# Performance work log

Hardware: AMD Instinct MI355X
Metric: run time of the kernel (lower is better)

## Reference

```python
import jax, jax.numpy as jnp
import numpy as np

N_NODES = 100000
N_EDGES = 3200000
IN_DIM = 128
OUT_DIM = 128
BN_EPS = 1e-5
FILL_VALUE = 1.0  # improved_gcn=False -> self-loop weight 1.0 (2.0 if improved)


def setup_inputs() -> dict:
    key = jax.random.key(0)
    k1, k2, k3, k4 = jax.random.split(key, 4)
    node_features = jax.random.normal(k1, (N_NODES, IN_DIM), dtype=jnp.float32)
    edge_index = jax.random.randint(k2, (2, N_EDGES), 0, N_NODES, dtype=jnp.int64)
    edge_weight = jax.random.uniform(k3, (N_EDGES,), dtype=jnp.float32)
    # Glorot init like PyG GCNConv
    W = jax.random.normal(k4, (IN_DIM, OUT_DIM), dtype=jnp.float32) * np.sqrt(2.0 / (IN_DIM + OUT_DIM))
    b = jnp.zeros((OUT_DIM,), dtype=jnp.float32)
    gamma = jnp.ones((OUT_DIM,), dtype=jnp.float32)
    beta = jnp.zeros((OUT_DIM,), dtype=jnp.float32)
    return {"node_features": node_features, "edge_index": edge_index,
            "edge_weight": edge_weight, "W": W, "b": b, "gamma": gamma, "beta": beta}


def reference(node_features, edge_index, edge_weight, W, b, gamma, beta):
    N = node_features.shape[0]
    dt = node_features.dtype
    # --- gcn_norm: add self loops, symmetric normalization ---
    loop = jnp.arange(N, dtype=edge_index.dtype)
    row = jnp.concatenate([edge_index[0], loop])  # source
    col = jnp.concatenate([edge_index[1], loop])  # target (aggregation dim)
    w = jnp.concatenate([edge_weight.astype(dt), jnp.full((N,), FILL_VALUE, dtype=dt)])
    deg = jax.ops.segment_sum(w, col, num_segments=N)
    dinv = jnp.where(deg > 0, jax.lax.rsqrt(deg), 0.0).astype(dt)
    norm = dinv[row] * w * dinv[col]  # [E+N]
    # --- linear transform then message passing (scatter-add into targets) ---
    x = node_features @ W  # [N, out_dim]
    msg = x[row] * norm[:, None]  # [E+N, out_dim] gather
    out = jax.ops.segment_sum(msg, col, num_segments=N) + b
    # --- relu ---
    h = jax.nn.relu(out)
    # --- BatchNorm1d (training-mode batch statistics, biased variance) ---
    mean = jnp.mean(h, axis=0)
    var = jnp.mean(jnp.square(h - mean), axis=0)
    h = (h - mean) * jax.lax.rsqrt(var + BN_EPS) * gamma + beta
    # dropout is identity in eval / deterministic reference
    return h
```

## Files before the change

kernel.cpp:

```cpp
#include <hip/hip_runtime.h>
#include <hip/hip_bf16.h>


#define BKT_BITS 7
#define BKT_SZ 128
#define MAX_BKT 1024
#define CHUNK 8192

typedef __attribute__((ext_vector_type(8))) short bf16x8;
typedef __attribute__((ext_vector_type(4))) float f32x4;

__device__ __forceinline__ unsigned bf16rn(float f) {
    unsigned x = __float_as_uint(f);
    return (x + 0x7fffu + ((x >> 16) & 1u)) >> 16;
}
__device__ __forceinline__ float bflo(unsigned u) { return __uint_as_float(u << 16); }
__device__ __forceinline__ float bfhi(unsigned u) { return __uint_as_float(u & 0xffff0000u); }

__global__ __launch_bounds__(256) void k_bhist2(const int* __restrict__ col,
        int* __restrict__ blkoff, const float* __restrict__ Wm,
        unsigned* __restrict__ WT, int E, int nb, int nbc) {
    __shared__ int h[MAX_BKT];
    for (int i = threadIdx.x; i < nb; i += 256) h[i] = 0;
    __syncthreads();
    int base = blockIdx.x * CHUNK, lim = min(base + CHUNK, E);
    for (int e = base + threadIdx.x; e < lim; e += 256)
        atomicAdd(&h[col[e] >> BKT_BITS], 1);
    __syncthreads();
    for (int i = threadIdx.x; i < nb; i += 256)
        blkoff[(size_t)i * nbc + blockIdx.x] = h[i];
    if (blockIdx.x == 0) {
        for (int i = threadIdx.x; i < 128 * 64; i += 256) {
            int j = i >> 6, w = i & 63;
            float a = Wm[(size_t)(2 * w) * 128 + j];
            float b = Wm[(size_t)(2 * w + 1) * 128 + j];
            WT[i] = bf16rn(a) | (bf16rn(b) << 16);
        }
    }
}

__global__ void k_bscan2a(int* __restrict__ blkoff, int* __restrict__ btot,
                          int nb, int nbc) {
    int b = blockIdx.x * 256 + threadIdx.x;
    if (b >= nb) return;
    int* p = blkoff + (size_t)b * nbc;
    int run = 0;
#pragma unroll 4
    for (int i = 0; i < nbc; ++i) { int c = p[i]; p[i] = run; run += c; }
    btot[b] = run;
}

__global__ __launch_bounds__(1024) void k_bscan2b(const int* __restrict__ btot,
        int* __restrict__ bbase, int* __restrict__ ptr, float* __restrict__ sums,
        int nb, int N, int E) {
    __shared__ int ls[1024];
    int t = threadIdx.x;
    int v = (t < nb) ? btot[t] : 0;
    ls[t] = v;
    __syncthreads();
    for (int off = 1; off < 1024; off <<= 1) {
        int u = (t >= off) ? ls[t - off] : 0;
        __syncthreads();
        ls[t] += u;
        __syncthreads();
    }
    if (t < nb) bbase[t] = ls[t] - v;
    if (t == nb - 1) bbase[nb] = ls[t];
    if (t == 0) ptr[N] = E;
    if (t < 512) sums[t] = 0.0f;
}

__global__ __launch_bounds__(256) void k_passA3(
        const int* __restrict__ row, const int* __restrict__ col,
        const float* __restrict__ w, const int* __restrict__ blkoff,
        const int* __restrict__ bbase, unsigned* __restrict__ tmp,
        int E, int nb, int nbc) {
    __shared__ int cur[MAX_BKT];
    for (int i = threadIdx.x; i < nb; i += 256)
        cur[i] = bbase[i] + blkoff[(size_t)i * nbc + blockIdx.x];
    __syncthreads();
    int base = blockIdx.x * CHUNK, lim = min(base + CHUNK, E);
    for (int e = base + threadIdx.x; e < lim; e += 256) {
        int c = col[e];
        int q8 = (int)(w[e] * 256.0f + 0.5f);
        if (q8 > 255) q8 = 255;
        unsigned rec = ((unsigned)row[e] << 15) | ((unsigned)(c & 127) << 8) | (unsigned)q8;
        int pos = atomicAdd(&cur[c >> BKT_BITS], 1);
        tmp[pos] = rec;
    }
}

__global__ __launch_bounds__(256) void k_passB2(
        const unsigned* __restrict__ tmp, const int* __restrict__ bbase,
        unsigned* __restrict__ packed, int* __restrict__ ptr,
        float* __restrict__ dinv, int N) {
    __shared__ int hcnt[BKT_SZ];
    __shared__ int wsumi[BKT_SZ];
    __shared__ int cur[BKT_SZ];
    __shared__ float dcl[BKT_SZ];
    int b = blockIdx.x;
    int t = threadIdx.x;
    if (t < BKT_SZ) { hcnt[t] = 0; wsumi[t] = 0; }
    __syncthreads();
    int beg = bbase[b], end = bbase[b + 1];
    for (int k = beg + t; k < end; k += 256) {
        unsigned p = tmp[k];
        int li = (p >> 8) & 127;
        atomicAdd(&hcnt[li], 1);
        atomicAdd(&wsumi[li], (int)(p & 255u));
    }
    __syncthreads();
    if (t < BKT_SZ) cur[t] = hcnt[t];
    __syncthreads();
    for (int off = 1; off < BKT_SZ; off <<= 1) {
        int v = (t < BKT_SZ && t >= off) ? cur[t - off] : 0;
        __syncthreads();
        if (t < BKT_SZ) cur[t] += v;
        __syncthreads();
    }
    if (t < BKT_SZ) {
        int p = beg + cur[t] - hcnt[t];
        cur[t] = p;
        float d = 1.0f + (float)wsumi[t] * (1.0f / 256.0f);
        float dc = rsqrtf(d);
        dcl[t] = dc;
        int n = (b << BKT_BITS) + t;
        if (n < N) { ptr[n] = p; dinv[n] = dc; }
    }
    __syncthreads();
    for (int k = beg + t; k < end; k += 256) {
        unsigned p = tmp[k];
        int li = (p >> 8) & 127;
        int pos = atomicAdd(&cur[li], 1);
        float fw = (float)(p & 255u) * (1.0f / 256.0f) * dcl[li];
        unsigned wb = bf16rn(fw) & 0x7FFFu;
        packed[pos] = ((p >> 15) << 15) | wb;
    }
}

__global__ void k_conv2(const float* __restrict__ nf, const float* __restrict__ dinv,
                        uint4* __restrict__ tab, int N) {
    size_t i = (size_t)blockIdx.x * 256 + threadIdx.x;
    if (i >= (size_t)N * 16) return;
    int n = (int)(i >> 4);
    float dv = dinv[n];
    const float4* src = (const float4*)nf + 2 * i;
    float4 a = src[0], b = src[1];
    uint4 r;
    r.x = bf16rn(a.x * dv) | (bf16rn(a.y * dv) << 16);
    r.y = bf16rn(a.z * dv) | (bf16rn(a.w * dv) << 16);
    r.z = bf16rn(b.x * dv) | (bf16rn(b.y * dv) << 16);
    r.w = bf16rn(b.z * dv) | (bf16rn(b.w * dv) << 16);
    tab[i] = r;
}

#define EDGE_FMA(aX, nX, tX)                                     \
    aX[0] += nX * bflo(tX.x); aX[1] += nX * bfhi(tX.x);          \
    aX[2] += nX * bflo(tX.y); aX[3] += nX * bfhi(tX.y);          \
    aX[4] += nX * bflo(tX.z); aX[5] += nX * bfhi(tX.z);          \
    aX[6] += nX * bflo(tX.w); aX[7] += nX * bfhi(tX.w);

__global__ __launch_bounds__(256) void k_gatherw5(
        const unsigned* __restrict__ packed, const int* __restrict__ ptr,
        const float* __restrict__ dinv, const unsigned* __restrict__ tab,
        unsigned* __restrict__ aggb, int N) {
    int wid = (int)(((size_t)blockIdx.x * 256 + threadIdx.x) >> 6);
    int lane = threadIdx.x & 63;
    if (wid >= N) return;
    int beg = ptr[wid], end = ptr[wid + 1];
    float dc = dinv[wid];
    int q = lane >> 4;
    int fl = lane & 15;
    float a0[8] = {}, a1[8] = {}, a2[8] = {}, a3[8] = {};
    int k = beg;
    for (; k + 16 <= end; k += 16) {
        unsigned p0 = packed[k + q];
        unsigned p1 = packed[k + 4 + q];
        unsigned p2 = packed[k + 8 + q];
        unsigned p3 = packed[k + 12 + q];
        uint4 t0 = *(const uint4*)(tab + (size_t)(p0 >> 15) * 64 + fl * 4);
        uint4 t1 = *(const uint4*)(tab + (size_t)(p1 >> 15) * 64 + fl * 4);
        uint4 t2 = *(const uint4*)(tab + (size_t)(p2 >> 15) * 64 + fl * 4);
        uint4 t3 = *(const uint4*)(tab + (size_t)(p3 >> 15) * 64 + fl * 4);
        float n0 = bflo(p0 & 0x7FFFu);
        float n1 = bflo(p1 & 0x7FFFu);
        float n2 = bflo(p2 & 0x7FFFu);
        float n3 = bflo(p3 & 0x7FFFu);
        EDGE_FMA(a0, n0, t0)
        EDGE_FMA(a1, n1, t1)
        EDGE_FMA(a2, n2, t2)
        EDGE_FMA(a3, n3, t3)
    }
    if (k + 8 <= end) {
        unsigned p0 = packed[k + q];
        unsigned p1 = packed[k + 4 + q];
        uint4 t0 = *(const uint4*)(tab + (size_t)(p0 >> 15) * 64 + fl * 4);
        uint4 t1 = *(const uint4*)(tab + (size_t)(p1 >> 15) * 64 + fl * 4);
        float n0 = bflo(p0 & 0x7FFFu);
        float n1 = bflo(p1 & 0x7FFFu);
        EDGE_FMA(a0, n0, t0)
        EDGE_FMA(a1, n1, t1)
        k += 8;
    }
    for (; k < end; k += 4) {
        int i0 = k + q;
        if (i0 < end) {
            unsigned p0 = packed[i0];
            uint4 t0 = *(const uint4*)(tab + (size_t)(p0 >> 15) * 64 + fl * 4);
            float n0 = bflo(p0 & 0x7FFFu);
            EDGE_FMA(a0, n0, t0)
        }
    }
#pragma unroll
    for (int j = 0; j < 8; ++j) {
        float s = (a0[j] + a1[j]) + (a2[j] + a3[j]);
        s += __shfl_xor(s, 16);
        s += __shfl_xor(s, 32);
        a0[j] = s;
    }
    if (q == 0) {
        uint4 t = *(const uint4*)(tab + (size_t)wid * 64 + fl * 4);
        EDGE_FMA(a0, dc, t)
        uint4 r;
        r.x = bf16rn(a0[0]) | (bf16rn(a0[1]) << 16);
        r.y = bf16rn(a0[2]) | (bf16rn(a0[3]) << 16);
        r.z = bf16rn(a0[4]) | (bf16rn(a0[5]) << 16);
        r.w = bf16rn(a0[6]) | (bf16rn(a0[7]) << 16);
        *(uint4*)(aggb + (size_t)wid * 64 + fl * 4) = r;
    }
}

__global__ __launch_bounds__(256) void k_gatherwF(
        const unsigned* __restrict__ packed, const int* __restrict__ ptr,
        const float* __restrict__ dinv, const unsigned* __restrict__ tab,
        float* __restrict__ out, int N) {
    int wid = (int)(((size_t)blockIdx.x * 256 + threadIdx.x) >> 6);
    int lane = threadIdx.x & 63;
    if (wid >= N) return;
    int beg = ptr[wid], end = ptr[wid + 1];
    float dc = dinv[wid];
    int q = lane >> 4;
    int fl = lane & 15;
    float a0[8] = {}, a1[8] = {};
    int k = beg;
    for (; k + 8 <= end; k += 8) {
        unsigned p0 = packed[k + q];
        unsigned p1 = packed[k + 4 + q];
        uint4 t0 = *(const uint4*)(tab + (size_t)(p0 >> 15) * 64 + fl * 4);
        uint4 t1 = *(const uint4*)(tab + (size_t)(p1 >> 15) * 64 + fl * 4);
        float n0 = bflo(p0 & 0x7FFFu);
        float n1 = bflo(p1 & 0x7FFFu);
        EDGE_FMA(a0, n0, t0)
        EDGE_FMA(a1, n1, t1)
    }
    for (; k < end; k += 4) {
        int i0 = k + q;
        if (i0 < end) {
            unsigned p0 = packed[i0];
            uint4 t0 = *(const uint4*)(tab + (size_t)(p0 >> 15) * 64 + fl * 4);
            float n0 = bflo(p0 & 0x7FFFu);
            EDGE_FMA(a0, n0, t0)
        }
    }
#pragma unroll
    for (int j = 0; j < 8; ++j) {
        float s = a0[j] + a1[j];
        s += __shfl_xor(s, 16);
        s += __shfl_xor(s, 32);
        a0[j] = s;
    }
    if (q == 0) {
        uint4 t = *(const uint4*)(tab + (size_t)wid * 64 + fl * 4);
        EDGE_FMA(a0, dc, t)
        float4* dst = (float4*)(out + (size_t)wid * 128 + fl * 8);
        dst[0] = make_float4(a0[0], a0[1], a0[2], a0[3]);
        dst[1] = make_float4(a0[4], a0[5], a0[6], a0[7]);
    }
}

__global__ __launch_bounds__(256) void k_gemm4(
        unsigned* aggb, const unsigned* __restrict__ WT,
        const float* __restrict__ bias, float* __restrict__ sums, int N) {
    __shared__ unsigned A_l[128][68];
    __shared__ float bs[256];
    int tid = threadIdx.x;
    int r0 = blockIdx.x * 128;
    bs[tid] = 0.0f;
    {
        int j = tid >> 1, h = tid & 1;
        int gr = r0 + j;
        if (gr < N) {
            const uint4* src = (const uint4*)(aggb + (size_t)gr * 64 + h * 32);
#pragma unroll
            for (int i = 0; i < 8; ++i)
                *(uint4*)&A_l[j][h * 32 + i * 4] = src[i];
        } else {
            uint4 z = {0, 0, 0, 0};
#pragma unroll
            for (int i = 0; i < 8; ++i)
                *(uint4*)&A_l[j][h * 32 + i * 4] = z;
        }
    }
    __syncthreads();

    int wv = tid >> 6, l = tid & 63;
    int lr = l & 15, lk = l >> 4;
    f32x4 acc[2][8] = {};
#pragma unroll
    for (int ks = 0; ks < 4; ++ks) {
        bf16x8 a0 = *(bf16x8*)&A_l[wv * 32 + lr][ks * 16 + lk * 4];
        bf16x8 a1 = *(bf16x8*)&A_l[wv * 32 + 16 + lr][ks * 16 + lk * 4];
#pragma unroll
        for (int nt = 0; nt < 8; ++nt) {
            bf16x8 b = *(const bf16x8*)(WT + (size_t)(nt * 16 + lr) * 64 + ks * 16 + lk * 4);
            acc[0][nt] = __builtin_amdgcn_mfma_f32_16x16x32_bf16(a0, b, acc[0][nt], 0, 0, 0);
            acc[1][nt] = __builtin_amdgcn_mfma_f32_16x16x32_bf16(a1, b, acc[1][nt], 0, 0, 0);
        }
    }

    unsigned short* ab = (unsigned short*)aggb;
#pragma unroll
    for (int nt = 0; nt < 8; ++nt) {
        int colc = nt * 16 + lr;
        float bc = bias[colc];
        float s = 0.0f, sq = 0.0f;
#pragma unroll
        for (int ms = 0; ms < 2; ++ms) {
#pragma unroll
            for (int p = 0; p < 4; ++p) {
                int rrow = r0 + wv * 32 + ms * 16 + lk * 4 + p;
                float v = fmaxf(acc[ms][nt][p] + bc, 0.0f);
                if (rrow < N) {
                    ab[(size_t)rrow * 128 + colc] = (unsigned short)bf16rn(v);
                    s += v;
                    sq += v * v;
                }
            }
        }
        s += __shfl_xor(s, 16);  s += __shfl_xor(s, 32);
        sq += __shfl_xor(sq, 16); sq += __shfl_xor(sq, 32);
        if (l < 16) {
            atomicAdd(&bs[colc], s);
            atomicAdd(&bs[128 + colc], sq);
        }
    }
    __syncthreads();
    if (tid < 128) {
        atomicAdd(&sums[tid], bs[tid]);
        atomicAdd(&sums[128 + tid], bs[128 + tid]);
    }
}

__global__ __launch_bounds__(256) void k_bnapplyB2(
        const unsigned* __restrict__ aggb, const float* __restrict__ sums,
        const float* __restrict__ gamma, const float* __restrict__ beta,
        float* __restrict__ out, size_t n16, int N) {
    __shared__ float sc[128], sh[128];
    int t = threadIdx.x;
    if (t < 128) {
        float inv_n = 1.0f / (float)N;
        float mean = sums[t] * inv_n;
        float var = sums[128 + t] * inv_n - mean * mean;
        float s = rsqrtf(var + 1e-5f) * gamma[t];
        sc[t] = s;
        sh[t] = beta[t] - mean * s;
    }
    __syncthreads();
    size_t i = (size_t)blockIdx.x * 256 + threadIdx.x;
    if (i >= n16) return;
    int g = (int)(i & 15);
    uint4 v = ((const uint4*)aggb)[i];
    float4 sc0 = *(float4*)&sc[g * 8];
    float4 sc1 = *(float4*)&sc[g * 8 + 4];
    float4 sh0 = *(float4*)&sh[g * 8];
    float4 sh1 = *(float4*)&sh[g * 8 + 4];
    float4 o0, o1;
    o0.x = bflo(v.x) * sc0.x + sh0.x;
    o0.y = bfhi(v.x) * sc0.y + sh0.y;
    o0.z = bflo(v.y) * sc0.z + sh0.z;
    o0.w = bfhi(v.y) * sc0.w + sh0.w;
    o1.x = bflo(v.z) * sc1.x + sh1.x;
    o1.y = bfhi(v.z) * sc1.y + sh1.y;
    o1.z = bflo(v.w) * sc1.z + sh1.z;
    o1.w = bfhi(v.w) * sc1.w + sh1.w;
    ((float4*)out)[2 * i] = o0;
    ((float4*)out)[2 * i + 1] = o1;
}

__global__ void k_bnfin(float* __restrict__ sums, const float* __restrict__ gamma,
                        const float* __restrict__ beta, int N) {
    int j = threadIdx.x;
    float inv_n = 1.0f / (float)N;
    float mean = sums[j] * inv_n;
    float var = sums[128 + j] * inv_n - mean * mean;
    float sc = rsqrtf(var + 1e-5f) * gamma[j];
    sums[256 + j] = sc;
    sums[384 + j] = beta[j] - mean * sc;
}

__global__ void k_bnapply(float* __restrict__ h, const float* __restrict__ sums, size_t n4) {
    size_t i = (size_t)blockIdx.x * 256 + threadIdx.x;
    if (i >= n4) return;
    int j4 = (int)(i & 31);
    float4 v = ((float4*)h)[i];
    float4 sc = ((const float4*)(sums + 256))[j4];
    float4 sh = ((const float4*)(sums + 384))[j4];
    v.x = v.x * sc.x + sh.x;
    v.y = v.y * sc.y + sh.y;
    v.z = v.z * sc.z + sh.z;
    v.w = v.w * sc.w + sh.w;
    ((float4*)h)[i] = v;
}

__global__ void k_init0(int* __restrict__ bcnt, float* __restrict__ sums, int nb) {
    int i = blockIdx.x * 256 + threadIdx.x;
    if (i < nb) bcnt[i] = 0;
    if (blockIdx.x == 0 && threadIdx.x < 512) sums[threadIdx.x] = 0.0f;
}
__global__ __launch_bounds__(256) void k_bhist(const int* __restrict__ col,
                                               int* __restrict__ bcnt, int E, int nb) {
    __shared__ int h[MAX_BKT];
    for (int i = threadIdx.x; i < nb; i += 256) h[i] = 0;
    __syncthreads();
    int base = blockIdx.x * CHUNK, lim = min(base + CHUNK, E);
    for (int e = base + threadIdx.x; e < lim; e += 256)
        atomicAdd(&h[col[e] >> BKT_BITS], 1);
    __syncthreads();
    for (int i = threadIdx.x; i < nb; i += 256) {
        int c = h[i];
        if (c) atomicAdd(&bcnt[i], c);
    }
}
__global__ __launch_bounds__(1024) void k_bscan(const int* __restrict__ bcnt,
        int* __restrict__ bbase, int* __restrict__ bcur,
        int* __restrict__ ptr, int nb, int N, int E) {
    __shared__ int ls[1024];
    int t = threadIdx.x;
    int v = (t < nb) ? bcnt[t] : 0;
    ls[t] = v;
    __syncthreads();
    for (int off = 1; off < 1024; off <<= 1) {
        int u = (t >= off) ? ls[t - off] : 0;
        __syncthreads();
        ls[t] += u;
        __syncthreads();
    }
    if (t < nb) {
        int ex = ls[t] - v;
        bbase[t] = ex;
        bcur[t] = ex;
    }
    if (t == nb - 1) bbase[nb] = ls[t];
    if (t == 0) ptr[N] = E;
}
__global__ __launch_bounds__(256) void k_passA2(
        const int* __restrict__ row, const int* __restrict__ col,
        const float* __restrict__ w, int* __restrict__ bcur,
        unsigned* __restrict__ tmp, int E, int nb) {
    __shared__ int h[MAX_BKT];
    for (int i = threadIdx.x; i < nb; i += 256) h[i] = 0;
    __syncthreads();
    int base = blockIdx.x * CHUNK, lim = min(base + CHUNK, E);
    for (int e = base + threadIdx.x; e < lim; e += 256)
        atomicAdd(&h[col[e] >> BKT_BITS], 1);
    __syncthreads();
    for (int i = threadIdx.x; i < nb; i += 256) {
        int c = h[i];
        if (c) h[i] = atomicAdd(&bcur[i], c);
    }
    __syncthreads();
    for (int e = base + threadIdx.x; e < lim; e += 256) {
        int c = col[e];
        int q8 = (int)(w[e] * 256.0f + 0.5f);
        if (q8 > 255) q8 = 255;
        unsigned rec = ((unsigned)row[e] << 15) | ((unsigned)(c & 127) << 8) | (unsigned)q8;
        int pos = atomicAdd(&h[c >> BKT_BITS], 1);
        tmp[pos] = rec;
    }
}

__global__ void k_init(int* __restrict__ cnt, float* __restrict__ sums, int N) {
    int i = blockIdx.x * 256 + threadIdx.x;
    if (i < N) cnt[i] = 0;
    if (blockIdx.x == 0 && threadIdx.x < 512) sums[threadIdx.x] = 0.0f;
}
__global__ void k_count(const int* __restrict__ col, int* __restrict__ cnt, int E) {
    int e = blockIdx.x * 256 + threadIdx.x;
    if (e < E) atomicAdd(&cnt[col[e]], 1);
}
__global__ __launch_bounds__(256) void kS1(const int* __restrict__ cnt,
                                           int* __restrict__ ptr,
                                           int* __restrict__ bsum, int N) {
    __shared__ int ls[256];
    int t = threadIdx.x, i = blockIdx.x * 256 + t;
    int v = (i < N) ? cnt[i] : 0;
    ls[t] = v;
    __syncthreads();
    for (int off = 1; off < 256; off <<= 1) {
        int u = (t >= off) ? ls[t - off] : 0;
        __syncthreads();
        ls[t] += u;
        __syncthreads();
    }
    if (i < N) ptr[i] = ls[t] - v;
    if (t == 255) bsum[blockIdx.x] = ls[255];
}
__global__ __launch_bounds__(512) void kS2(int* __restrict__ bsum,
                                           int* __restrict__ ptr, int NB, int N) {
    __shared__ int ls[512];
    int t = threadIdx.x;
    int chunk = (NB + 511) / 512;
    int b = t * chunk, e = min(b + chunk, NB);
    int s = 0;
    for (int i = b; i < e; ++i) s += bsum[i];
    ls[t] = s;
    __syncthreads();
    for (int off = 1; off < 512; off <<= 1) {
        int u = (t >= off) ? ls[t - off] : 0;
        __syncthreads();
        ls[t] += u;
        __syncthreads();
    }
    int run = ls[t] - s;
    for (int i = b; i < e; ++i) { int c = bsum[i]; bsum[i] = run; run += c; }
    if (t == 511) ptr[N] = ls[511];
}
__global__ void kS3(int* __restrict__ ptr, int* __restrict__ cnt,
                    const int* __restrict__ bsum, int N) {
    int i = blockIdx.x * 256 + threadIdx.x;
    if (i >= N) return;
    int p = ptr[i] + bsum[blockIdx.x];
    ptr[i] = p;
    cnt[i] = p;
}
__global__ void k_fill(const int* __restrict__ row, const int* __restrict__ col,
                       const float* __restrict__ w, int* __restrict__ cursor,
                       int2* __restrict__ packed, int E) {
    int e = blockIdx.x * 256 + threadIdx.x;
    if (e < E) {
        int pos = atomicAdd(&cursor[col[e]], 1);
        packed[pos] = make_int2(row[e], __float_as_int(w[e]));
    }
}
__global__ __launch_bounds__(256) void k_degw(const int2* __restrict__ packed,
                                              const int* __restrict__ ptr,
                                              float* __restrict__ dinv, int N) {
    int wid = (int)(((size_t)blockIdx.x * 256 + threadIdx.x) >> 6);
    int lane = threadIdx.x & 63;
    if (wid >= N) return;
    int beg = ptr[wid], end = ptr[wid + 1];
    float s = 0.0f;
    for (int k = beg + lane; k < end; k += 64) s += __int_as_float(packed[k].y);
#pragma unroll
    for (int off = 32; off; off >>= 1) s += __shfl_xor(s, off);
    if (lane == 0) {
        float d = 1.0f + s;
        dinv[wid] = d > 0.0f ? rsqrtf(d) : 0.0f;
    }
}
__global__ __launch_bounds__(256) void k_gather(
        const int2* __restrict__ packed, const int* __restrict__ ptr,
        const float* __restrict__ dinv, const float* __restrict__ nf,
        float* __restrict__ out, int N) {
    int wid = (int)(((size_t)blockIdx.x * 256 + threadIdx.x) >> 6);
    int lane = threadIdx.x & 63;
    if (wid >= N) return;
    int c = wid;
    int beg = ptr[c], end = ptr[c + 1];
    float dc = dinv[c];
    int half = lane >> 5;
    int fl = lane & 31;
    float4 acc = {0.f, 0.f, 0.f, 0.f};
    for (int k = beg; k < end; k += 2) {
        int idx = k + half;
        bool v = idx < end;
        int2 p = packed[v ? idx : beg];
        float nrm = v ? dc * __int_as_float(p.y) * dinv[p.x] : 0.0f;
        float4 x = ((const float4*)(nf + (size_t)p.x * 128))[fl];
        acc.x += nrm * x.x; acc.y += nrm * x.y;
        acc.z += nrm * x.z; acc.w += nrm * x.w;
    }
    acc.x += __shfl_xor(acc.x, 32);
    acc.y += __shfl_xor(acc.y, 32);
    acc.z += __shfl_xor(acc.z, 32);
    acc.w += __shfl_xor(acc.w, 32);
    if (half == 0) {
        float s2 = dc * dc;
        float4 sf = ((const float4*)(nf + (size_t)c * 128))[fl];
        acc.x += s2 * sf.x; acc.y += s2 * sf.y;
        acc.z += s2 * sf.z; acc.w += s2 * sf.w;
        ((float4*)(out + (size_t)c * 128))[fl] = acc;
    }
}
__global__ void k_initA(float* __restrict__ deg, float* __restrict__ sums, int N) {
    int i = blockIdx.x * 256 + threadIdx.x;
    if (i < N) deg[i] = 1.0f;
    if (blockIdx.x == 0 && threadIdx.x < 512) sums[threadIdx.x] = 0.0f;
}
__global__ void k_deg(const int* __restrict__ col, const float* __restrict__ w,
                      float* __restrict__ deg, int E) {
    int e = blockIdx.x * 256 + threadIdx.x;
    if (e < E) atomicAdd(&deg[col[e]], w[e]);
}
__global__ void k_dinv(float* __restrict__ deg, int N) {
    int i = blockIdx.x * 256 + threadIdx.x;
    if (i < N) { float d = deg[i]; deg[i] = d > 0.0f ? rsqrtf(d) : 0.0f; }
}
__global__ void k_self(const float* __restrict__ nf, const float* __restrict__ dinv,
                       float* __restrict__ agg, int N) {
    size_t i = (size_t)blockIdx.x * 256 + threadIdx.x;
    if (i >= (size_t)N * 32) return;
    int node = (int)(i >> 5);
    float s = dinv[node]; s = s * s;
    float4 v = ((const float4*)nf)[i];
    v.x *= s; v.y *= s; v.z *= s; v.w *= s;
    ((float4*)agg)[i] = v;
}
__global__ __launch_bounds__(256) void k_scatter(
        const int* __restrict__ row, const int* __restrict__ col,
        const float* __restrict__ w, const float* __restrict__ dinv,
        const float* __restrict__ nf, float* __restrict__ agg, int E) {
    int wid = (int)(((size_t)blockIdx.x * blockDim.x + threadIdx.x) >> 6);
    int lane = threadIdx.x & 63;
    if (wid >= E) return;
    int r = row[wid], c = col[wid];
    float nrm = dinv[r] * w[wid] * dinv[c];
    float2 v = ((const float2*)(nf + (size_t)r * 128))[lane];
    float* dst = agg + (size_t)c * 128 + lane * 2;
    atomicAdd(dst, v.x * nrm);
    atomicAdd(dst + 1, v.y * nrm);
}

__global__ __launch_bounds__(256) void k_gemm2(float* __restrict__ h,
        const float* __restrict__ W, const float* __restrict__ bias,
        float* __restrict__ sums, int N) {
    __shared__ float At[2][32][132];
    __shared__ float Wt[2][32][132];
    int tid = threadIdx.x;
    int tx = tid & 15, ty = tid >> 4;
    int r0 = blockIdx.x * 128;
#define STAGE_A(buf, k0)                                                     \
    _Pragma("unroll")                                                        \
    for (int i = 0; i < 4; ++i) {                                            \
        int idx = tid + 256 * i;                                             \
        int row = idx >> 3, c4 = idx & 7;                                    \
        int gr = r0 + row; if (gr > N - 1) gr = N - 1;                       \
        float4 v = *(const float4*)&h[(size_t)gr * 128 + (k0) + c4 * 4];     \
        At[buf][c4 * 4 + 0][row] = v.x;                                      \
        At[buf][c4 * 4 + 1][row] = v.y;                                      \
        At[buf][c4 * 4 + 2][row] = v.z;                                      \
        At[buf][c4 * 4 + 3][row] = v.w;                                      \
    }
#define STAGE_W(buf, k0)                                                     \
    _Pragma("unroll")                                                        \
    for (int i = 0; i < 4; ++i) {                                            \
        int idx = tid + 256 * i;                                             \
        int kk = idx >> 5, c4 = idx & 31;                                    \
        float4 v = *(const float4*)&W[(size_t)((k0) + kk) * 128 + c4 * 4];   \
        *(float4*)&Wt[buf][kk][c4 * 4] = v;                                  \
    }
    STAGE_A(0, 0)
    STAGE_W(0, 0)
    float acc[8][8] = {};
    for (int t = 0; t < 4; ++t) {
        __syncthreads();
        if (t < 3) {
            int nb = (t + 1) & 1;
            STAGE_A(nb, (t + 1) * 32)
            STAGE_W(nb, (t + 1) * 32)
        }
        int kb = t & 1;
#pragma unroll
        for (int k = 0; k < 32; ++k) {
            float a[8], w[8];
            *(float4*)&a[0] = *(float4*)&At[kb][k][ty * 8];
            *(float4*)&a[4] = *(float4*)&At[kb][k][ty * 8 + 4];
            *(float4*)&w[0] = *(float4*)&Wt[kb][k][tx * 8];
            *(float4*)&w[4] = *(float4*)&Wt[kb][k][tx * 8 + 4];
#pragma unroll
            for (int r = 0; r < 8; ++r)
#pragma unroll
                for (int cc = 0; cc < 8; ++cc)
                    acc[r][cc] += a[r] * w[cc];
        }
    }
    float bv[8];
    *(float4*)&bv[0] = *(const float4*)&bias[tx * 8];
    *(float4*)&bv[4] = *(const float4*)&bias[tx * 8 + 4];
    float s[8] = {}, sq[8] = {};
#pragma unroll
    for (int r = 0; r < 8; ++r) {
        int gr = r0 + ty * 8 + r;
        if (gr < N) {
            float o[8];
#pragma unroll
            for (int cc = 0; cc < 8; ++cc) {
                o[cc] = fmaxf(acc[r][cc] + bv[cc], 0.0f);
                s[cc] += o[cc];
                sq[cc] += o[cc] * o[cc];
            }
            float4* dst = (float4*)&h[(size_t)gr * 128 + tx * 8];
            dst[0] = make_float4(o[0], o[1], o[2], o[3]);
            dst[1] = make_float4(o[4], o[5], o[6], o[7]);
        }
    }
    float* ls = &At[0][0][0];
    __syncthreads();
#pragma unroll
    for (int cc = 0; cc < 8; ++cc) {
        ls[ty * 128 + tx * 8 + cc] = s[cc];
        ls[2048 + ty * 128 + tx * 8 + cc] = sq[cc];
    }
    __syncthreads();
    if (tid < 128) {
        float ssum = 0.f, sqsum = 0.f;
#pragma unroll
        for (int u = 0; u < 16; ++u) {
            ssum += ls[u * 128 + tid];
            sqsum += ls[2048 + u * 128 + tid];
        }
        atomicAdd(&sums[tid], ssum);
        atomicAdd(&sums[128 + tid], sqsum);
    }
#undef STAGE_A
#undef STAGE_W
}

extern "C" void kernel_launch(void* const* d_in, const int* in_sizes, int n_in,
                              void* d_out, int out_size, void* d_ws, size_t ws_size,
                              hipStream_t stream) {
    const float* nf    = (const float*)d_in[0];
    const int*   ei    = (const int*)d_in[1];
    const float* ew    = (const float*)d_in[2];
    const float* W     = (const float*)d_in[3];
    const float* bias  = (const float*)d_in[4];
    const float* gamma = (const float*)d_in[5];
    const float* beta  = (const float*)d_in[6];
    float* out = (float*)d_out;

    const int N = in_sizes[0] / 128;
    const int E = in_sizes[2];
    const int* row = ei;
    const int* col = ei + E;

    int nb_n  = (N + 255) / 256;
    int nb_e  = (E + 255) / 256;
    int nb_w  = (int)(((size_t)N + 3) / 4);
    int nb_v4 = (int)(((size_t)N * 32 + 255) / 256);
    int nbk   = (N + BKT_SZ - 1) >> BKT_BITS;
    int nb_c  = (E + CHUNK - 1) / CHUNK;
    int nconv = (int)(((size_t)N * 16 + 255) / 256);
    size_t n16 = (size_t)N * 16;
    size_t tt_words = (size_t)64 * N > (size_t)E ? (size_t)64 * N : (size_t)E;

    float* dinv = (float*)d_ws;
    int*   ptr  = (int*)d_ws + N;
    float* sums = (float*)d_ws + 2 * N + 1;
    int*   bbase1 = (int*)d_ws + 2 * N + 513;
    int*   btot   = bbase1 + nbk + 1;
    int*   blkoff = btot + nbk;
    size_t wt_off = ((size_t)(2 * N + 514 + 2 * nbk) + (size_t)nbk * nb_c + 3) & ~(size_t)3;
    unsigned* wtb = (unsigned*)((int*)d_ws + wt_off);
    size_t pk_off = (wt_off + 8192 + 3) & ~(size_t)3;
    unsigned* p1_packed = (unsigned*)((int*)d_ws + pk_off);
    size_t tt_off = (pk_off + (size_t)E + 3) & ~(size_t)3;
    unsigned* p1_tmp = (unsigned*)((int*)d_ws + tt_off);
    unsigned* p1_tab = (unsigned*)((int*)d_ws + tt_off);
    size_t ab_off = (tt_off + tt_words + 3) & ~(size_t)3;
    unsigned* aggb = (unsigned*)((int*)d_ws + ab_off);
    size_t need_p1 = (ab_off + (size_t)64 * N) * 4;

    float* dinv2 = (float*)d_ws;
    int*   ptr2  = (int*)d_ws + N;
    int*   cnt3  = (int*)d_ws + 2 * N + 1;
    float* sums2 = (float*)d_ws + 3 * N + 1;
    int*   bsum2 = (int*)d_ws + 3 * N + 513;
    int*   bbase2 = (int*)d_ws + 3 * N + 1025;
    int*   bcur2  = bbase2 + nbk + 1;
    size_t pk2 = ((size_t)(3 * N + 1026 + 2 * nbk) + 3) & ~(size_t)3;
    unsigned* packed2 = (unsigned*)((int*)d_ws + pk2);
    size_t tt2 = (pk2 + (size_t)E + 3) & ~(size_t)3;
    unsigned* tmp2 = (unsigned*)((int*)d_ws + tt2);
    unsigned* tab2 = (unsigned*)((int*)d_ws + tt2);
    size_t need_full2 = (tt2 + tt_words) * 4;

    int2*  packed3 = (int2*)((int*)d_ws + pk2);
    size_t need_csr3 = (pk2 + (size_t)2 * E) * 4;

    if (nbk <= MAX_BKT && ws_size >= need_p1) {
        k_bhist2<<<nb_c, 256, 0, stream>>>(col, blkoff, W, wtb, E, nbk, nb_c);
        k_bscan2a<<<(nbk + 255) / 256, 256, 0, stream>>>(blkoff, btot, nbk, nb_c);
        k_bscan2b<<<1, 1024, 0, stream>>>(btot, bbase1, ptr, sums, nbk, N, E);
        k_passA3<<<nb_c, 256, 0, stream>>>(row, col, ew, blkoff, bbase1, p1_tmp, E, nbk, nb_c);
        k_passB2<<<nbk, 256, 0, stream>>>(p1_tmp, bbase1, p1_packed, ptr, dinv, N);
        k_conv2<<<nconv, 256, 0, stream>>>(nf, dinv, (uint4*)p1_tab, N);
        k_gatherw5<<<nb_w, 256, 0, stream>>>(p1_packed, ptr, dinv, p1_tab, aggb, N);
        k_gemm4<<<(N + 127) / 128, 256, 0, stream>>>(aggb, wtb, bias, sums, N);
        k_bnapplyB2<<<(int)((n16 + 255) / 256), 256, 0, stream>>>(aggb, sums, gamma, beta, out, n16, N);
        return;
    }

    if (nbk <= MAX_BKT && ws_size >= need_full2) {
        k_init0<<<(max(nbk, 512) + 255) / 256, 256, 0, stream>>>(bcur2, sums2, nbk);
        k_bhist<<<nb_c, 256, 0, stream>>>(col, bcur2, E, nbk);
        k_bscan<<<1, 1024, 0, stream>>>(bcur2, bbase2, bcur2, ptr2, nbk, N, E);
        k_passA2<<<nb_c, 256, 0, stream>>>(row, col, ew, bcur2, tmp2, E, nbk);
        k_passB2<<<nbk, 256, 0, stream>>>(tmp2, bbase2, packed2, ptr2, dinv2, N);
        k_conv2<<<nconv, 256, 0, stream>>>(nf, dinv2, (uint4*)tab2, N);
        k_gatherwF<<<nb_w, 256, 0, stream>>>(packed2, ptr2, dinv2, tab2, out, N);
        k_gemm2<<<(N + 127) / 128, 256, 0, stream>>>(out, W, bias, sums2, N);
        k_bnfin<<<1, 128, 0, stream>>>(sums2, gamma, beta, N);
        k_bnapply<<<nb_v4, 256, 0, stream>>>(out, sums2, (size_t)N * 32);
        return;
    }

    if (ws_size >= need_csr3) {
        k_init<<<nb_n, 256, 0, stream>>>(cnt3, sums2, N);
        k_count<<<nb_e, 256, 0, stream>>>(col, cnt3, E);
        kS1<<<nb_n, 256, 0, stream>>>(cnt3, ptr2, bsum2, N);
        kS2<<<1, 512, 0, stream>>>(bsum2, ptr2, nb_n, N);
        kS3<<<nb_n, 256, 0, stream>>>(ptr2, cnt3, bsum2, N);
        k_fill<<<nb_e, 256, 0, stream>>>(row, col, ew, cnt3, packed3, E);
        k_degw<<<nb_w, 256, 0, stream>>>(packed3, ptr2, dinv2, N);
        k_gather<<<nb_w, 256, 0, stream>>>(packed3, ptr2, dinv2, nf, out, N);
        k_gemm2<<<(N + 127) / 128, 256, 0, stream>>>(out, W, bias, sums2, N);
        k_bnfin<<<1, 128, 0, stream>>>(sums2, gamma, beta, N);
        k_bnapply<<<nb_v4, 256, 0, stream>>>(out, sums2, (size_t)N * 32);
        return;
    }

    {
        float* deg = (float*)d_ws;
        float* sm  = (float*)d_ws + N;
        k_initA<<<nb_n, 256, 0, stream>>>(deg, sm, N);
        k_deg<<<nb_e, 256, 0, stream>>>(col, ew, deg, E);
        k_dinv<<<nb_n, 256, 0, stream>>>(deg, N);
        k_self<<<nb_v4, 256, 0, stream>>>(nf, deg, out, N);
        k_scatter<<<(E + 3) / 4, 256, 0, stream>>>(row, col, ew, deg, nf, out, E);
        k_gemm2<<<(N + 127) / 128, 256, 0, stream>>>(out, W, bias, sm, N);
        k_bnfin<<<1, 128, 0, stream>>>(sm, gamma, beta, N);
        k_bnapply<<<nb_v4, 256, 0, stream>>>(out, sm, (size_t)N * 32);
    }
}
```

Baseline: 339.1 us.

## Fuse bf16 feature conversion into bucket CSR pass and stage W in LDS

Adds k_passB3, which builds the per-bucket CSR and degree normalization and then, in the same block, scales and converts that bucket's node features to bf16. This removes the separate k_conv2 launch and its extra read of dinv. The converted table goes into a separate workspace region when there is room, presumably so it no longer aliases the temp buffer still being read. The GEMM kernel now loads the transposed W into shared memory once per block instead of reading it from global memory inside the MFMA loop, at the cost of an extra 35 KB of LDS per block, which may lower occupancy.

Result: faster. 324.0 us (-4.5%).

```diff
diff --git a/kernel.cpp b/kernel.cpp
--- a/kernel.cpp
+++ b/kernel.cpp
@@ -87,6 +87,71 @@
         unsigned rec = ((unsigned)row[e] << 15) | ((unsigned)(c & 127) << 8) | (unsigned)q8;
         int pos = atomicAdd(&cur[c >> BKT_BITS], 1);
         tmp[pos] = rec;
+    }
+}
+
+__global__ __launch_bounds__(256) void k_passB3(
+        const unsigned* __restrict__ tmp, const int* __restrict__ bbase,
+        const float* __restrict__ nf, unsigned* __restrict__ tab,
+        unsigned* __restrict__ packed, int* __restrict__ ptr,
+        float* __restrict__ dinv, int N) {
+    __shared__ int hcnt[BKT_SZ];
+    __shared__ int wsumi[BKT_SZ];
+    __shared__ int cur[BKT_SZ];
+    __shared__ float dcl[BKT_SZ];
+    int b = blockIdx.x;
+    int t = threadIdx.x;
+    int node0 = b << BKT_BITS;
+    if (t < BKT_SZ) { hcnt[t] = 0; wsumi[t] = 0; }
+    __syncthreads();
+    int beg = bbase[b], end = bbase[b + 1];
+    for (int k = beg + t; k < end; k += 256) {
+        unsigned p = tmp[k];
+        int li = (p >> 8) & 127;
+        atomicAdd(&hcnt[li], 1);
+        atomicAdd(&wsumi[li], (int)(p & 255u));
+    }
+    __syncthreads();
+    if (t < BKT_SZ) cur[t] = hcnt[t];
+    __syncthreads();
+    for (int off = 1; off < BKT_SZ; off <<= 1) {
+        int v = (t < BKT_SZ && t >= off) ? cur[t - off] : 0;
+        __syncthreads();
+        if (t < BKT_SZ) cur[t] += v;
+        __syncthreads();
+    }
+    if (t < BKT_SZ) {
+        int p = beg + cur[t] - hcnt[t];
+        cur[t] = p;
+        float d = 1.0f + (float)wsumi[t] * (1.0f / 256.0f);
+        float dc = rsqrtf(d);
+        dcl[t] = dc;
+        int n = node0 + t;
+        if (n < N) { ptr[n] = p; dinv[n] = dc; }
+    }
+    __syncthreads();
+    for (int k = beg + t; k < end; k += 256) {
+        unsigned p = tmp[k];
+        int li = (p >> 8) & 127;
+        int pos = atomicAdd(&cur[li], 1);
+        float fw = (float)(p & 255u) * (1.0f / 256.0f) * dcl[li];
+        unsigned wb = bf16rn(fw) & 0x7FFFu;
+        packed[pos] = ((p >> 15) << 15) | wb;
+    }
+    for (int i = t; i < BKT_SZ * 16; i += 256) {
+        int r = i >> 4, q4 = i & 15;
+        int n = node0 + r;
+        if (n < N) {
+            float dv = dcl[r];
+            const float4* src = (const float4*)(nf + (size_t)n * 128 + q4 * 8);
+            float4 a = src[0], bb = src[1];
+            uint4 rr;
+            rr.x = bf16rn(a.x * dv) | (bf16rn(a.y * dv) << 16);
+            rr.y = bf16rn(a.z * dv) | (bf16rn(a.w * dv) << 16);
+            rr.z = bf16rn(bb.x * dv) | (bf16rn(bb.y * dv) << 16);
+            rr.w = bf16rn(bb.z * dv) | (bf16rn(bb.w * dv) << 16);
+            *(uint4*)(tab + (size_t)n * 64 + q4 * 4) = rr;
+        }
     }
 }
 
@@ -278,16 +343,24 @@
     }
 }
 
-__global__ __launch_bounds__(256) void k_gemm4(
+__global__ __launch_bounds__(256) void k_gemm3b(
         unsigned* aggb, const unsigned* __restrict__ WT,
         const float* __restrict__ bias, float* __restrict__ sums, int N) {
     __shared__ unsigned A_l[128][68];
+    __shared__ unsigned W_l[128][68];
     __shared__ float bs[256];
     int tid = threadIdx.x;
     int r0 = blockIdx.x * 128;
     bs[tid] = 0.0f;
     {
         int j = tid >> 1, h = tid & 1;
+        const uint4* src = (const uint4*)(WT + j * 64 + h * 32);
+#pragma unroll
+        for (int i = 0; i < 8; ++i)
+            *(uint4*)&W_l[j][h * 32 + i * 4] = src[i];
+    }
+    {
+        int j = tid >> 1, h = tid & 1;
         int gr = r0 + j;
         if (gr < N) {
             const uint4* src = (const uint4*)(aggb + (size_t)gr * 64 + h * 32);
@@ -312,7 +385,7 @@
         bf16x8 a1 = *(bf16x8*)&A_l[wv * 32 + 16 + lr][ks * 16 + lk * 4];
 #pragma unroll
         for (int nt = 0; nt < 8; ++nt) {
-            bf16x8 b = *(const bf16x8*)(WT + (size_t)(nt * 16 + lr) * 64 + ks * 16 + lk * 4);
+            bf16x8 b = *(bf16x8*)&W_l[nt * 16 + lr][ks * 16 + lk * 4];
             acc[0][nt] = __builtin_amdgcn_mfma_f32_16x16x32_bf16(a0, b, acc[0][nt], 0, 0, 0);
             acc[1][nt] = __builtin_amdgcn_mfma_f32_16x16x32_bf16(a1, b, acc[1][nt], 0, 0, 0);
         }
@@ -788,14 +861,26 @@
     size_t need_csr3 = (pk2 + (size_t)2 * E) * 4;
 
     if (nbk <= MAX_BKT && ws_size >= need_p1) {
-        k_bhist2<<<nb_c, 256, 0, stream>>>(col, blkoff, W, wtb, E, nbk, nb_c);
-        k_bscan2a<<<(nbk + 255) / 256, 256, 0, stream>>>(blkoff, btot, nbk, nb_c);
-        k_bscan2b<<<1, 1024, 0, stream>>>(btot, bbase1, ptr, sums, nbk, N, E);
-        k_passA3<<<nb_c, 256, 0, stream>>>(row, col, ew, blkoff, bbase1, p1_tmp, E, nbk, nb_c);
-        k_passB2<<<nbk, 256, 0, stream>>>(p1_tmp, bbase1, p1_packed, ptr, dinv, N);
-        k_conv2<<<nconv, 256, 0, stream>>>(nf, dinv, (uint4*)p1_tab, N);
-        k_gatherw5<<<nb_w, 256, 0, stream>>>(p1_packed, ptr, dinv, p1_tab, aggb, N);
-        k_gemm4<<<(N + 127) / 128, 256, 0, stream>>>(aggb, wtb, bias, sums, N);
+        unsigned* tab_sep = aggb + (size_t)64 * N;
+        size_t need_sep = (ab_off + (size_t)128 * N) * 4;
+        unsigned* tab_use = (ws_size >= need_sep) ? tab_sep : p1_tab;
+        if (ws_size >= need_sep) {
+            k_bhist2<<<nb_c, 256, 0, stream>>>(col, blkoff, W, wtb, E, nbk, nb_c);
+            k_bscan2a<<<(nbk + 255) / 256, 256, 0, stream>>>(blkoff, btot, nbk, nb_c);
+            k_bscan2b<<<1, 1024, 0, stream>>>(btot, bbase1, ptr, sums, nbk, N, E);
+            k_passA3<<<nb_c, 256, 0, stream>>>(row, col, ew, blkoff, bbase1, p1_tmp, E, nbk, nb_c);
+            k_passB3<<<nbk, 256, 0, stream>>>(p1_tmp, bbase1, nf, tab_use, p1_packed, ptr, dinv, N);
+            k_gatherw5<<<nb_w, 256, 0, stream>>>(p1_packed, ptr, dinv, tab_use, aggb, N);
+        } else {
+            k_bhist2<<<nb_c, 256, 0, stream>>>(col, blkoff, W, wtb, E, nbk, nb_c);
+            k_bscan2a<<<(nbk + 255) / 256, 256, 0, stream>>>(blkoff, btot, nbk, nb_c);
+            k_bscan2b<<<1, 1024, 0, stream>>>(btot, bbase1, ptr, sums, nbk, N, E);
+            k_passA3<<<nb_c, 256, 0, stream>>>(row, col, ew, blkoff, bbase1, p1_tmp, E, nbk, nb_c);
+            k_passB2<<<nbk, 256, 0, stream>>>(p1_tmp, bbase1, p1_packed, ptr, dinv, N);
+            k_conv2<<<nconv, 256, 0, stream>>>(nf, dinv, (uint4*)p1_tab, N);
+            k_gatherw5<<<nb_w, 256, 0, stream>>>(p1_packed, ptr, dinv, p1_tab, aggb, N);
+        }
+        k_gemm3b<<<(N + 127) / 128, 256, 0, stream>>>(aggb, wtb, bias, sums, N);
         k_bnapplyB2<<<(int)((n16 + 255) / 256), 256, 0, stream>>>(aggb, sums, gamma, beta, out, n16, N);
         return;
     }
```
